# Kernel optimization log

Measured on AMD Instinct MI355X. Metric: run time of the kernel, lower is better.

The kernel has to match this reference:

```python
import jax, jax.numpy as jnp
import numpy as np
import math

RES = 2048
EGG_FACTOR = 0.25
BUMP_STRENGTH = 1.0
SPEC_POWER = 32.0
AMBIENT = 0.1
_L = np.array([0.5, 0.7, 1.0], dtype=np.float32)
LIGHT = _L / np.sqrt((_L * _L).sum())
VIEW = np.array([0.0, 0.0, 1.0], dtype=np.float32)
F0 = np.float32(((1.5 - 1.0) / (1.5 + 1.0)) ** 2)  # Schlick F0 from IOR=1.5 -> 0.04


def _pixel_grid():
    # matches torch.meshgrid(x, y, indexing='xy') ray generation buffers
    x = np.arange(RES, dtype=np.float32)
    y = np.arange(RES, dtype=np.float32)
    px, py = np.meshgrid(x, y, indexing='xy')
    scale = 0.85
    nx = (px / RES - 0.5) * 2.0 / scale
    ny = (0.5 - py / RES) * 2.0 / scale
    return jnp.asarray(nx), jnp.asarray(ny)


def sample_bilinear(tex, u, v):
    # BilinearSampler with UV wrap; tex: (H, W, C), u/v: (...,)
    h, w = tex.shape[0], tex.shape[1]
    u = u % 1.0
    v = v % 1.0
    x = u * w - 0.5
    y = v * h - 0.5
    x0 = jnp.floor(x).astype(jnp.int32) % w
    y0 = jnp.floor(y).astype(jnp.int32) % h
    x1 = (x0 + 1) % w
    y1 = (y0 + 1) % h
    fx = (x - jnp.floor(x))[..., None]
    fy = (y - jnp.floor(y))[..., None]
    v00 = tex[y0, x0]
    v01 = tex[y0, x1]
    v10 = tex[y1, x0]
    v11 = tex[y1, x1]
    return (v00 * (1 - fx) * (1 - fy) + v01 * fx * (1 - fy)
            + v10 * (1 - fx) * fy + v11 * fx * fy)


def _tbn(n):
    # Gram-Schmidt tangent frame from surface normal field, (..., 3)
    up = jnp.zeros_like(n).at[..., 1].set(1.0)
    right = jnp.zeros_like(n).at[..., 0].set(1.0)
    dot_up = n[..., 1]
    ref = jnp.where((jnp.abs(dot_up) > 0.99)[..., None], right, up)
    t = ref - jnp.sum(ref * n, axis=-1, keepdims=True) * n
    t = t / jnp.clip(jnp.linalg.norm(t, axis=-1, keepdims=True), 1e-6)
    b = jnp.cross(n, t)
    return t, b


def reference(texture, normal_map):
    nx, ny = _pixel_grid()
    # 1-2. ray-sphere intersection
    r_sq = nx * nx + ny * ny
    inside = r_sq <= 1.0
    z = jnp.sqrt(jnp.clip(1.0 - r_sq, 0.0))
    # 3. egg deformation
    egg_mod = 1.0 - EGG_FACTOR * ny
    safe = jnp.abs(egg_mod) > 0.01
    x_egg = jnp.where(safe, nx / egg_mod, nx)
    z_egg = jnp.where(safe, z / egg_mod, z)
    # 4. spherical UV
    phi = jnp.arccos(jnp.clip(ny, -1.0, 1.0))
    theta = jnp.arctan2(z_egg, x_egg)
    u = (theta / (2.0 * math.pi) + 0.5) % 1.0
    v = phi / math.pi
    # 5. texture / normal-map sampling
    albedo = sample_bilinear(texture, u, v)
    tex_n = sample_bilinear(normal_map, u, v) * 2.0 - 1.0  # [0,1] -> [-1,1]
    # 6. analytical egg normal + TBN frame
    sn = jnp.stack([nx * egg_mod, ny, z * egg_mod], axis=-1)
    base_n = sn / jnp.clip(jnp.linalg.norm(sn, axis=-1, keepdims=True), 1e-6)
    tangent, bitangent = _tbn(base_n)
    # 7. normal perturbation
    world_n = (tex_n[..., 0:1] * tangent + tex_n[..., 1:2] * bitangent
               + tex_n[..., 2:3] * base_n)
    nrm = base_n * (1.0 - BUMP_STRENGTH) + world_n * BUMP_STRENGTH
    nrm = nrm / jnp.clip(jnp.linalg.norm(nrm, axis=-1, keepdims=True), 1e-6)
    # 8. Blinn-Phong + Schlick Fresnel lighting
    light = jnp.asarray(LIGHT)
    view = jnp.asarray(VIEW)
    half = light + view
    half = half / jnp.linalg.norm(half)
    ndotl = jnp.clip(jnp.sum(nrm * light, axis=-1), 0.0)
    ndoth = jnp.clip(jnp.sum(nrm * half, axis=-1), 0.0)
    spec = ndoth ** SPEC_POWER
    ndotv = jnp.clip(jnp.sum(nrm * view, axis=-1), 0.0)
    fres = F0 + (1.0 - F0) * (1.0 - ndotv) ** 5
    color = albedo * (AMBIENT + ndotl)[..., None] + (spec * fres)[..., None]
    color = jnp.clip(color, 0.0, 1.0)
    return jnp.where(inside[..., None], color, 0.0)


def setup_inputs():
    key = jax.random.key(0)
    k1, k2 = jax.random.split(key)
    texture = jax.random.uniform(k1, (1024, 1024, 3), dtype=jnp.float32)
    normal_map = jax.random.uniform(k2, (1024, 1024, 3), dtype=jnp.float32)
    return {"texture": texture, "normal_map": normal_map}
```

## Files before the change

### kernel.cpp

```cpp
#include <hip/hip_runtime.h>
#include <math.h>

#define RESN 2048
#define TEXW 1024

__device__ __forceinline__ float fatan2_pos(float y, float x) {
    float ax = fabsf(x);
    float mn = fminf(ax, y);
    float mx = fmaxf(ax, y);
    float r0 = __builtin_amdgcn_rcpf(mx);
    r0 = r0 * __builtin_fmaf(-mx, r0, 2.0f);
    float a = mn * r0;
    bool red = a > 0.41421356f;
    float t = (a - 1.0f) * __builtin_amdgcn_rcpf(a + 1.0f);
    float w = red ? t : a;
    float s = w * w;
    float p = __builtin_fmaf(s, 8.05374449538e-2f, -1.38776856032e-1f);
    p = __builtin_fmaf(s, p, 1.99777106478e-1f);
    p = __builtin_fmaf(s, p, -3.33329491539e-1f);
    float r = __builtin_fmaf(w * s, p, w);
    r = red ? r + 0.78539816339f : r;
    r = (y > ax) ? 1.57079632679f - r : r;
    r = (x < 0.0f) ? 3.14159265359f - r : r;
    return r;
}

struct __align__(4) F3 { float x, y, z; };

__global__ __launch_bounds__(256, 8) void egg_render(
    const float* __restrict__ tex,
    const float* __restrict__ nmap,
    float* __restrict__ out)
{
    int p = blockIdx.x * 256 + threadIdx.x;
    int i = p & (RESN - 1);
    int j = p >> 11;
    float* o = out + (size_t)p * 3u;

    const float invres = 1.0f / (float)RESN;
    float nx = __fmul_rn(__fsub_rn(__fmul_rn((float)i, invres), 0.5f), 2.0f) / 0.85f;
    float ny = __fmul_rn(__fsub_rn(0.5f, __fmul_rn((float)j, invres)), 2.0f) / 0.85f;
    float rsq = __fadd_rn(__fmul_rn(nx, nx), __fmul_rn(ny, ny));
    if (!(rsq <= 1.0f)) {
        o[0] = 0.0f; o[1] = 0.0f; o[2] = 0.0f;
        return;
    }

    float z = sqrtf(fmaxf(__fsub_rn(1.0f, rsq), 0.0f));
    float egg = 1.0f - 0.25f * ny;

    float sphi = sqrtf(fmaxf(__builtin_fmaf(-ny, ny, 1.0f), 0.0f));
    float phi = fatan2_pos(sphi, ny);
    float v = phi * 0.3183098861837907f;

    float theta = fatan2_pos(z, nx);
    float u = theta * 0.15915494309189535f + 0.5f;

    float yy = v * (float)TEXW - 0.5f;
    float yf = floorf(yy);
    float fy = yy - yf;
    float gy = 1.0f - fy;
    int y0 = (int)yf & (TEXW - 1);
    int y1 = (y0 + 1) & (TEXW - 1);
    float xx = u * (float)TEXW - 0.5f;
    float xf = floorf(xx);
    float fx = xx - xf;
    float gx = 1.0f - fx;
    int x0 = (int)xf & (TEXW - 1);
    int x1 = (x0 + 1) & (TEXW - 1);
    float w00 = gx * gy, w01 = fx * gy, w10 = gx * fy, w11 = fx * fy;
    int o00 = (y0 * TEXW + x0) * 3;
    int o01 = (y0 * TEXW + x1) * 3;
    int o10 = (y1 * TEXW + x0) * 3;
    int o11 = (y1 * TEXW + x1) * 3;

    F3 a00 = *(const F3*)(tex + o00);
    F3 a01 = *(const F3*)(tex + o01);
    F3 a10 = *(const F3*)(tex + o10);
    F3 a11 = *(const F3*)(tex + o11);
    F3 n00 = *(const F3*)(nmap + o00);
    F3 n01 = *(const F3*)(nmap + o01);
    F3 n10 = *(const F3*)(nmap + o10);
    F3 n11 = *(const F3*)(nmap + o11);

    float ar = a00.x*w00 + a01.x*w01 + a10.x*w10 + a11.x*w11;
    float ag = a00.y*w00 + a01.y*w01 + a10.y*w10 + a11.y*w11;
    float ab = a00.z*w00 + a01.z*w01 + a10.z*w10 + a11.z*w11;
    float tnx = (n00.x*w00 + n01.x*w01 + n10.x*w10 + n11.x*w11) * 2.0f - 1.0f;
    float tny = (n00.y*w00 + n01.y*w01 + n10.y*w10 + n11.y*w11) * 2.0f - 1.0f;
    float tnz = (n00.z*w00 + n01.z*w01 + n10.z*w10 + n11.z*w11) * 2.0f - 1.0f;

    float snx = nx * egg, sny = ny, snz = z * egg;
    float sl2 = snx*snx + sny*sny + snz*snz;
    float isl = __builtin_amdgcn_rsqf(sl2);
    float bnx = snx * isl, bny = sny * isl, bnz = snz * isl;

    bool use_right = fabsf(bny) > 0.99f;
    float d = use_right ? bnx : bny;
    float m = use_right ? bny : bnx;
    float q2 = m * m + bnz * bnz;
    float iq = __builtin_amdgcn_rsqf(q2);
    float q  = q2 * iq;
    float e  = -(d * iq);
    float tz = bnz * e;
    float txc = bnx * e;
    float tyr = bny * e;
    float tx = use_right ? q   : txc;
    float ty = use_right ? tyr : q;
    float bnxiq = bnx * iq, bnyiq = bny * iq, bnziq = bnz * iq;
    float bx = use_right ? 0.0f   : -bnziq;
    float by = use_right ? bnziq  : 0.0f;
    float bz = use_right ? -bnyiq : bnxiq;

    float wx = tnx * tx + tny * bx + tnz * bnx;
    float wy = tnx * ty + tny * by + tnz * bny;
    float wz = tnx * tz + tny * bz + tnz * bnz;
    float wl2 = wx*wx + wy*wy + wz*wz;
    float iwl = __builtin_amdgcn_rsqf(fmaxf(wl2, 1e-12f));
    wx *= iwl; wy *= iwl; wz *= iwl;

    float Lx = 0.5f, Ly = 0.7f, Lz = 1.0f;
    float ll = sqrtf(Lx * Lx + Ly * Ly + Lz * Lz);
    Lx /= ll; Ly /= ll; Lz /= ll;
    float Hx = Lx, Hy = Ly, Hz = Lz + 1.0f;
    float hl = sqrtf(Hx * Hx + Hy * Hy + Hz * Hz);
    Hx /= hl; Hy /= hl; Hz /= hl;

    float ndotl = fmaxf(wx * Lx + wy * Ly + wz * Lz, 0.0f);
    float ndoth = fmaxf(wx * Hx + wy * Hy + wz * Hz, 0.0f);
    float s2 = ndoth * ndoth, s4 = s2 * s2, s8 = s4 * s4, s16 = s8 * s8;
    float spec = s16 * s16;
    float ndotv = fmaxf(wz, 0.0f);
    float t1 = 1.0f - ndotv;
    float t2 = t1 * t1, t4 = t2 * t2;
    float fres = 0.04f + 0.96f * (t4 * t1);
    float ka = 0.1f + ndotl;
    float add = spec * fres;

    o[0] = fminf(fmaxf(__builtin_fmaf(ar, ka, add), 0.0f), 1.0f);
    o[1] = fminf(fmaxf(__builtin_fmaf(ag, ka, add), 0.0f), 1.0f);
    o[2] = fminf(fmaxf(__builtin_fmaf(ab, ka, add), 0.0f), 1.0f);
}

extern "C" void kernel_launch(void* const* d_in, const int* in_sizes, int n_in,
                              void* d_out, int out_size, void* d_ws, size_t ws_size,
                              hipStream_t stream) {
    const float* tex  = (const float*)d_in[0];
    const float* nmap = (const float*)d_in[1];
    float* out = (float*)d_out;
    int total = RESN * RESN;
    dim3 grid(total / 256), block(256);
    hipLaunchKernelGGL(egg_render, grid, block, 0, stream, tex, nmap, out);
}
```

Baseline: 28.45 us.

## Stage the two texture rows per image row in LDS, one block per row

Each block now renders one image row with 512 threads covering 4 pixels each. It hoists the row-invariant v/y computation and preloads the two needed texture and normal-map rows (the half that theta can reach) into shared memory as float4. The eight scattered 12-byte global gathers per pixel become LDS reads. In exchange it adds a cooperative load, a barrier and LDS usage per block. Pixels outside the disk now do the full shading work and are masked at the end.

```diff
diff --git a/kernel.cpp b/kernel.cpp
--- a/kernel.cpp
+++ b/kernel.cpp
@@ -25,99 +25,49 @@
     return r;
 }
 
-struct __align__(4) F3 { float x, y, z; };
-
-__global__ __launch_bounds__(256, 8) void egg_render(
+__global__ __launch_bounds__(512) void egg_render(
     const float* __restrict__ tex,
     const float* __restrict__ nmap,
     float* __restrict__ out)
 {
-    int p = blockIdx.x * 256 + threadIdx.x;
-    int i = p & (RESN - 1);
-    int j = p >> 11;
-    float* o = out + (size_t)p * 3u;
+    int j = blockIdx.x;
+    int tid = threadIdx.x;
+    float* orow = out + (size_t)j * RESN * 3u;
 
     const float invres = 1.0f / (float)RESN;
-    float nx = __fmul_rn(__fsub_rn(__fmul_rn((float)i, invres), 0.5f), 2.0f) / 0.85f;
     float ny = __fmul_rn(__fsub_rn(0.5f, __fmul_rn((float)j, invres)), 2.0f) / 0.85f;
-    float rsq = __fadd_rn(__fmul_rn(nx, nx), __fmul_rn(ny, ny));
-    if (!(rsq <= 1.0f)) {
-        o[0] = 0.0f; o[1] = 0.0f; o[2] = 0.0f;
+    float nysq = __fmul_rn(ny, ny);
+
+    if (!(nysq <= 1.0f)) {
+        #pragma unroll
+        for (int k = 0; k < 4; ++k) {
+            float* o = orow + ((k << 9) + tid) * 3;
+            o[0] = 0.f; o[1] = 0.f; o[2] = 0.f;
+        }
         return;
     }
 
-    float z = sqrtf(fmaxf(__fsub_rn(1.0f, rsq), 0.0f));
     float egg = 1.0f - 0.25f * ny;
-
     float sphi = sqrtf(fmaxf(__builtin_fmaf(-ny, ny, 1.0f), 0.0f));
     float phi = fatan2_pos(sphi, ny);
     float v = phi * 0.3183098861837907f;
-
-    float theta = fatan2_pos(z, nx);
-    float u = theta * 0.15915494309189535f + 0.5f;
-
     float yy = v * (float)TEXW - 0.5f;
     float yf = floorf(yy);
     float fy = yy - yf;
     float gy = 1.0f - fy;
     int y0 = (int)yf & (TEXW - 1);
     int y1 = (y0 + 1) & (TEXW - 1);
-    float xx = u * (float)TEXW - 0.5f;
-    float xf = floorf(xx);
-    float fx = xx - xf;
-    float gx = 1.0f - fx;
-    int x0 = (int)xf & (TEXW - 1);
-    int x1 = (x0 + 1) & (TEXW - 1);
-    float w00 = gx * gy, w01 = fx * gy, w10 = gx * fy, w11 = fx * fy;
-    int o00 = (y0 * TEXW + x0) * 3;
-    int o01 = (y0 * TEXW + x1) * 3;
-    int o10 = (y1 * TEXW + x0) * 3;
-    int o11 = (y1 * TEXW + x1) * 3;
 
-    F3 a00 = *(const F3*)(tex + o00);
-    F3 a01 = *(const F3*)(tex + o01);
-    F3 a10 = *(const F3*)(tex + o10);
-    F3 a11 = *(const F3*)(tex + o11);
-    F3 n00 = *(const F3*)(nmap + o00);
-    F3 n01 = *(const F3*)(nmap + o01);
-    F3 n10 = *(const F3*)(nmap + o10);
-    F3 n11 = *(const F3*)(nmap + o11);
-
-    float ar = a00.x*w00 + a01.x*w01 + a10.x*w10 + a11.x*w11;
-    float ag = a00.y*w00 + a01.y*w01 + a10.y*w10 + a11.y*w11;
-    float ab = a00.z*w00 + a01.z*w01 + a10.z*w10 + a11.z*w11;
-    float tnx = (n00.x*w00 + n01.x*w01 + n10.x*w10 + n11.x*w11) * 2.0f - 1.0f;
-    float tny = (n00.y*w00 + n01.y*w01 + n10.y*w10 + n11.y*w11) * 2.0f - 1.0f;
-    float tnz = (n00.z*w00 + n01.z*w01 + n10.z*w10 + n11.z*w11) * 2.0f - 1.0f;
-
-    float snx = nx * egg, sny = ny, snz = z * egg;
-    float sl2 = snx*snx + sny*sny + snz*snz;
-    float isl = __builtin_amdgcn_rsqf(sl2);
-    float bnx = snx * isl, bny = sny * isl, bnz = snz * isl;
-
-    bool use_right = fabsf(bny) > 0.99f;
-    float d = use_right ? bnx : bny;
-    float m = use_right ? bny : bnx;
-    float q2 = m * m + bnz * bnz;
-    float iq = __builtin_amdgcn_rsqf(q2);
-    float q  = q2 * iq;
-    float e  = -(d * iq);
-    float tz = bnz * e;
-    float txc = bnx * e;
-    float tyr = bny * e;
-    float tx = use_right ? q   : txc;
-    float ty = use_right ? tyr : q;
-    float bnxiq = bnx * iq, bnyiq = bny * iq, bnziq = bnz * iq;
-    float bx = use_right ? 0.0f   : -bnziq;
-    float by = use_right ? bnziq  : 0.0f;
-    float bz = use_right ? -bnyiq : bnxiq;
-
-    float wx = tnx * tx + tny * bx + tnz * bnx;
-    float wy = tnx * ty + tny * by + tnz * bny;
-    float wz = tnx * tz + tny * bz + tnz * bnz;
-    float wl2 = wx*wx + wy*wy + wz*wz;
-    float iwl = __builtin_amdgcn_rsqf(fmaxf(wl2, 1e-12f));
-    wx *= iwl; wy *= iwl; wz *= iwl;
+    __shared__ float4 lds[4][516];
+    for (int f = tid; f < 4 * 514; f += 512) {
+        int mr = f >> 9;
+        mr = f / 514;
+        int c = f - mr * 514;
+        int sy = (mr & 1) ? y1 : y0;
+        const float* src = ((mr & 2) ? nmap : tex) + ((sy << 10) + ((c + 511) & (TEXW - 1))) * 3;
+        lds[mr][c] = make_float4(src[0], src[1], src[2], 0.0f);
+    }
+    __syncthreads();
 
     float Lx = 0.5f, Ly = 0.7f, Lz = 1.0f;
     float ll = sqrtf(Lx * Lx + Ly * Ly + Lz * Lz);
@@ -126,20 +76,78 @@
     float hl = sqrtf(Hx * Hx + Hy * Hy + Hz * Hz);
     Hx /= hl; Hy /= hl; Hz /= hl;
 
-    float ndotl = fmaxf(wx * Lx + wy * Ly + wz * Lz, 0.0f);
-    float ndoth = fmaxf(wx * Hx + wy * Hy + wz * Hz, 0.0f);
-    float s2 = ndoth * ndoth, s4 = s2 * s2, s8 = s4 * s4, s16 = s8 * s8;
-    float spec = s16 * s16;
-    float ndotv = fmaxf(wz, 0.0f);
-    float t1 = 1.0f - ndotv;
-    float t2 = t1 * t1, t4 = t2 * t2;
-    float fres = 0.04f + 0.96f * (t4 * t1);
-    float ka = 0.1f + ndotl;
-    float add = spec * fres;
+    #pragma unroll
+    for (int k = 0; k < 4; ++k) {
+        int i = (k << 9) + tid;
+        float* o = orow + (size_t)i * 3u;
 
-    o[0] = fminf(fmaxf(__builtin_fmaf(ar, ka, add), 0.0f), 1.0f);
-    o[1] = fminf(fmaxf(__builtin_fmaf(ag, ka, add), 0.0f), 1.0f);
-    o[2] = fminf(fmaxf(__builtin_fmaf(ab, ka, add), 0.0f), 1.0f);
+        float nx = __fmul_rn(__fsub_rn(__fmul_rn((float)i, invres), 0.5f), 2.0f) / 0.85f;
+        float rsq = __fadd_rn(__fmul_rn(nx, nx), nysq);
+        bool ins = (rsq <= 1.0f);
+        float z = sqrtf(fmaxf(__fsub_rn(1.0f, rsq), 0.0f));
+
+        float theta = fatan2_pos(z, nx);
+        float u = theta * 0.15915494309189535f + 0.5f;
+        float xx = u * (float)TEXW - 0.5f;
+        float xf = floorf(xx);
+        float fx = xx - xf;
+        float gx = 1.0f - fx;
+        int rx = min(max((int)xf - 511, 0), 512);
+        float w00 = gx * gy, w01 = fx * gy, w10 = gx * fy, w11 = fx * fy;
+
+        float4 t00 = lds[0][rx], t01 = lds[0][rx + 1];
+        float4 t10 = lds[1][rx], t11 = lds[1][rx + 1];
+        float4 n00 = lds[2][rx], n01 = lds[2][rx + 1];
+        float4 n10 = lds[3][rx], n11 = lds[3][rx + 1];
+
+        float ar = t00.x*w00 + t01.x*w01 + t10.x*w10 + t11.x*w11;
+        float ag = t00.y*w00 + t01.y*w01 + t10.y*w10 + t11.y*w11;
+        float ab = t00.z*w00 + t01.z*w01 + t10.z*w10 + t11.z*w11;
+        float tnx = (n00.x*w00 + n01.x*w01 + n10.x*w10 + n11.x*w11) * 2.0f - 1.0f;
+        float tny = (n00.y*w00 + n01.y*w01 + n10.y*w10 + n11.y*w11) * 2.0f - 1.0f;
+        float tnz = (n00.z*w00 + n01.z*w01 + n10.z*w10 + n11.z*w11) * 2.0f - 1.0f;
+
+        float snx = nx * egg, sny = ny, snz = z * egg;
+        float sl2 = snx*snx + sny*sny + snz*snz;
+        float isl = __builtin_amdgcn_rsqf(sl2);
+        float bnx = snx * isl, bny = sny * isl, bnz = snz * isl;
+
+        bool use_right = fabsf(bny) > 0.99f;
+        float d = use_right ? bnx : bny;
+        float m = use_right ? bny : bnx;
+        float q2 = m * m + bnz * bnz;
+        float iq = __builtin_amdgcn_rsqf(q2);
+        float q  = q2 * iq;
+        float e  = -(d * iq);
+        float tzv = bnz * e;
+        float tx = use_right ? q : (bnx * e);
+        float ty = use_right ? (bny * e) : q;
+        float bx = use_right ? 0.0f        : -(bnz * iq);
+        float by = use_right ? (bnz * iq)  : 0.0f;
+        float bz = use_right ? -(bny * iq) : (bnx * iq);
+
+        float wx = tnx * tx + tny * bx + tnz * bnx;
+        float wy = tnx * ty + tny * by + tnz * bny;
+        float wz = tnx * tzv + tny * bz + tnz * bnz;
+        float wl2 = wx*wx + wy*wy + wz*wz;
+        float iwl = __builtin_amdgcn_rsqf(fmaxf(wl2, 1e-12f));
+        wx *= iwl; wy *= iwl; wz *= iwl;
+
+        float ndotl = fmaxf(wx * Lx + wy * Ly + wz * Lz, 0.0f);
+        float ndoth = fmaxf(wx * Hx + wy * Hy + wz * Hz, 0.0f);
+        float s2 = ndoth * ndoth, s4 = s2 * s2, s8 = s4 * s4, s16 = s8 * s8;
+        float spec = s16 * s16;
+        float ndotv = fmaxf(wz, 0.0f);
+        float t1 = 1.0f - ndotv;
+        float t2 = t1 * t1, t4 = t2 * t2;
+        float fres = 0.04f + 0.96f * (t4 * t1);
+        float ka = 0.1f + ndotl;
+        float add = spec * fres;
+
+        o[0] = ins ? fminf(fmaxf(__builtin_fmaf(ar, ka, add), 0.0f), 1.0f) : 0.0f;
+        o[1] = ins ? fminf(fmaxf(__builtin_fmaf(ag, ka, add), 0.0f), 1.0f) : 0.0f;
+        o[2] = ins ? fminf(fmaxf(__builtin_fmaf(ab, ka, add), 0.0f), 1.0f) : 0.0f;
+    }
 }
 
 extern "C" void kernel_launch(void* const* d_in, const int* in_sizes, int n_in,
@@ -148,7 +156,6 @@
     const float* tex  = (const float*)d_in[0];
     const float* nmap = (const float*)d_in[1];
     float* out = (float*)d_out;
-    int total = RESN * RESN;
-    dim3 grid(total / 256), block(256);
-    hipLaunchKernelGGL(egg_render, grid, block, 0, stream, tex, nmap, out);
+    hipLaunchKernelGGL(egg_render, dim3(RESN), dim3(512), 0, stream,
+                       tex, nmap, out);
 }
```

Measured after the change: 28.53 us. About the same (+0.3%).
